# Optimization experiments

Measured on AMD Instinct MI355X. Metric: run time of the kernel, lower is better.

## Reference

```python
import jax, jax.numpy as jnp
import numpy as np

B, S, D, H, E = 4, 2048, 512, 8, 4  # batch, seq, embed, heads, expand
HD = D // H


def setup_inputs() -> dict:
    key = jax.random.key(0)
    ks = jax.random.split(key, 9)
    s = lambda k, shape, fan: jax.random.normal(k, shape, jnp.float32) * (fan ** -0.5)
    return {
        "x": jax.random.normal(ks[0], (B, S, D), jnp.float32),
        "Wq": s(ks[1], (D, D), D),
        "Wk": s(ks[2], (D, D), D),
        "Wv": s(ks[3], (D, D), D),
        "Wo": s(ks[4], (D, D), D),
        "W1": s(ks[5], (D, D * E), D),
        "b1": jnp.zeros((D * E,), jnp.float32),
        "W2": s(ks[6], (D * E, D), D * E),
        "b2": jnp.zeros((D,), jnp.float32),
    }


def _encoder_layer(x, Wq, Wk, Wv, Wo, W1, b1, W2, b2):
    # NOTE: source computes InstanceNorm1d twice but discards both results -> no-ops.
    scale = D ** -0.25  # applied to BOTH q and k (net 1/sqrt(embed_dim))
    q = (x @ Wq).reshape(B, S, H, HD).transpose(0, 2, 1, 3) * scale  # [B,H,S,hd]
    k = (x @ Wk).reshape(B, S, H, HD).transpose(0, 2, 1, 3) * scale
    v = (x @ Wv).reshape(B, S, H, HD).transpose(0, 2, 1, 3)
    scores = jnp.einsum('bhqd,bhkd->bhqk', q, k)  # [B,H,S,S]
    attn = jax.nn.softmax(scores, axis=-1)
    o = jnp.einsum('bhqk,bhkd->bhqd', attn, v)  # [B,H,S,hd]
    o = o.transpose(0, 2, 1, 3).reshape(B, S, D)
    x = o @ Wo + x  # residual 1
    h = jax.nn.gelu(x @ W1 + b1, approximate=True)  # torch GELU(approximate='tanh')
    return h @ W2 + b2 + x  # residual 2 (dropout=0, eval)


def reference(x, Wq, Wk, Wv, Wo, W1, b1, W2, b2):
    return _encoder_layer(x, Wq, Wk, Wv, Wo, W1, b1, W2, b2)
```

## Files before the change

### kernel.cpp

```cpp
#include <hip/hip_runtime.h>
#include <hip/hip_bf16.h>


typedef __bf16 bf16;
typedef __attribute__((ext_vector_type(8))) __bf16 bf16x8;
typedef __attribute__((ext_vector_type(4))) __bf16 bf16x4;
typedef __attribute__((ext_vector_type(4))) float f32x4;
typedef __attribute__((ext_vector_type(16))) float f32x16;
typedef __attribute__((ext_vector_type(2))) unsigned int u32x2;
typedef __attribute__((ext_vector_type(4))) unsigned int u32x4;

#define LOG2E 1.4426950408889634f
#define SCORE_SCALE 0.044194173824159216f
#define SCALE_L2E (SCORE_SCALE * LOG2E)
#define FIXED_M 12.0f

#if __has_builtin(__builtin_amdgcn_exp2f)
#define EXP2(x) __builtin_amdgcn_exp2f(x)
#else
#define EXP2(x) exp2f(x)
#endif

__device__ __forceinline__ void gl_lds16(const bf16* g, bf16* l) {
  __builtin_amdgcn_global_load_lds(
      (const __attribute__((address_space(1))) unsigned int*)g,
      (__attribute__((address_space(3))) unsigned int*)l, 16, 0, 0);
}

template <int N>
__device__ __forceinline__ void wait_vm_barrier() {
  if constexpr (N == 0)
    asm volatile("s_waitcnt vmcnt(0)\ns_barrier" ::: "memory");
  else if constexpr (N == 3)
    asm volatile("s_waitcnt vmcnt(3)\ns_barrier" ::: "memory");
  else if constexpr (N == 4)
    asm volatile("s_waitcnt vmcnt(4)\ns_barrier" ::: "memory");
}

__device__ __forceinline__ float gelu_tanh(float x) {
  float u = 0.7978845608028654f * (x + 0.044715f * x * x * x);
  float e = EXP2(u * (2.0f * LOG2E));
  float th = 1.0f - 2.0f / (e + 1.0f);
  return 0.5f * x * (1.0f + th);
}

__device__ __forceinline__ f32x4 mfma_bf16(bf16x8 a, bf16x8 b, f32x4 c) {
  return __builtin_amdgcn_mfma_f32_16x16x32_bf16(a, b, c, 0, 0, 0);
}
__device__ __forceinline__ f32x16 mfma32x16(bf16x8 a, bf16x8 b, f32x16 c) {
  return __builtin_amdgcn_mfma_f32_32x32x16_bf16(a, b, c, 0, 0, 0);
}

__device__ __forceinline__ void plswap(unsigned int& a, unsigned int& b) {
  asm volatile("v_permlane32_swap_b32 %0, %1" : "+v"(a), "+v"(b));
}

template <int MODE, typename OutT, int TN>
__global__ __launch_bounds__(256, 2) void gemm_bt(
    const bf16* __restrict__ A, const bf16* __restrict__ Bt,
    OutT* __restrict__ C, const float* __restrict__ bias,
    const float* __restrict__ resf, const bf16* __restrict__ resb,
    int M, int N, int K) {
  constexpr int MI = (TN == 128) ? 4 : 2;
  constexpr int L = (TN == 128) ? 4 : 3;
  __shared__ __align__(16) bf16 sA[3][128 * 32];
  __shared__ __align__(16) bf16 sB[3][TN * 32];
  const int tid = threadIdx.x;
  const int lane = tid & 63;
  const int quad = lane >> 4, lc = lane & 15;
  const int wave = tid >> 6;
  const int wr = (TN == 128) ? (wave >> 1) : wave;
  const int wc = (TN == 128) ? (wave & 1) : 0;
  const int m0 = blockIdx.y * 128, n0 = blockIdx.x * TN;

  const int srow = tid >> 2;
  const int kc = (tid & 3) * 8;
  const bf16* Ag1 = A + (size_t)(m0 + srow) * K + kc;
  const bf16* Ag2 = A + (size_t)(m0 + 64 + srow) * K + kc;
  const bf16* Bg1 = Bt + (size_t)(n0 + srow) * K + kc;
  const bf16* Bg2 = Bt + (size_t)(n0 + 64 + srow) * K + kc;
  const int o1 = tid * 8, o2 = (tid + 256) * 8;

  f32x4 acc[MI][4];
#pragma unroll
  for (int mi = 0; mi < MI; ++mi)
#pragma unroll
    for (int ni = 0; ni < 4; ++ni) acc[mi][ni] = (f32x4){0.f, 0.f, 0.f, 0.f};

  auto stage = [&](int t) {
    bf16* a = sA[t % 3];
    bf16* bb = sB[t % 3];
    gl_lds16(Ag1 + t * 32, a + o1);
    gl_lds16(Ag2 + t * 32, a + o2);
    gl_lds16(Bg1 + t * 32, bb + o1);
    if (TN == 128) gl_lds16(Bg2 + t * 32, bb + o2);
  };

  const int kIters = K >> 5;
  stage(0);
  stage(1);

  for (int kt = 0; kt < kIters; ++kt) {
    if (kt + 1 < kIters)
      wait_vm_barrier<L>();
    else
      wait_vm_barrier<0>();
    if (kt + 2 < kIters) stage(kt + 2);
    const bf16* cA = sA[kt % 3];
    const bf16* cB = sB[kt % 3];

    bf16x8 af[MI], bfm[4];
#pragma unroll
    for (int i = 0; i < MI; ++i)
      af[i] =
          *(const bf16x8*)(cA + ((wr * (16 * MI) + i * 16 + lc) * 32 + quad * 8));
#pragma unroll
    for (int i = 0; i < 4; ++i)
      bfm[i] = *(const bf16x8*)(cB + ((wc * 64 + i * 16 + lc) * 32 + quad * 8));
#pragma unroll
    for (int mi = 0; mi < MI; ++mi)
#pragma unroll
      for (int ni = 0; ni < 4; ++ni)
        acc[mi][ni] = mfma_bf16(af[mi], bfm[ni], acc[mi][ni]);
  }

#pragma unroll
  for (int mi = 0; mi < MI; ++mi) {
#pragma unroll
    for (int r = 0; r < 4; ++r) {
      const int row = m0 + wr * (16 * MI) + mi * 16 + quad * 4 + r;
#pragma unroll
      for (int ni = 0; ni < 4; ++ni) {
        const int col = n0 + wc * 64 + ni * 16 + lc;
        const size_t idx = (size_t)row * N + col;
        float v = acc[mi][ni][r];
        if (MODE == 1) v += resf[idx];
        if (MODE == 2) v = gelu_tanh(v + bias[col]);
        if (MODE == 3) v += bias[col] + (float)resb[idx];
        C[idx] = (OutT)v;
      }
    }
  }
}

__global__ __launch_bounds__(256, 2) void flash_attn(
    const bf16* __restrict__ QKV, const bf16* __restrict__ Vt,
    bf16* __restrict__ O) {
  const int tid = threadIdx.x;
  const int lane = tid & 63, wave = tid >> 6;
  const int lo5 = lane & 31, hi = lane >> 5;
  const int lin = blockIdx.y * 16 + blockIdx.x;
  const int xcd = lin & 7, slot = lin >> 3;
  const int bh = xcd * 4 + (slot >> 4);
  const int qt = slot & 15;
  const int b = bh >> 3, h = bh & 7;
  const int q0 = qt * 128 + wave * 32;

  __shared__ __align__(16) bf16 sK[3][4096];
  __shared__ __align__(16) bf16 sV[3][4096];

  const bf16* Qrow = QKV + (size_t)(b * 2048 + q0 + lo5) * 1536 + h * 64;
  bf16x8 qf[4];
#pragma unroll
  for (int i = 0; i < 4; ++i) qf[i] = *(const bf16x8*)(Qrow + i * 16 + hi * 8);

  const int colsw = (((lane & 7) ^ (lane >> 3)) << 3);
  const bf16* Kg0 = QKV + (size_t)b * 2048 * 1536 + 512 + (size_t)h * 64 +
                    (size_t)(wave * 16 + (lane >> 3)) * 1536 + colsw;
  const bf16* Vg0 = Vt + (size_t)bh * 64 * 2048 +
                    (size_t)(wave * 16 + (lane >> 3)) * 2048 + colsw;
  const int stag = wave * 1024;
  const int m7 = lo5 & 7;

  f32x16 oacc[2];
  oacc[0] = (f32x16)(0.f);
  oacc[1] = (f32x16)(0.f);
  float rs0 = 0.f, rs1 = 0.f, rs2 = 0.f, rs3 = 0.f;

  auto stage = [&](int t) {
    bf16* dk = sK[t % 3] + stag;
    bf16* dv = sV[t % 3] + stag;
    gl_lds16(Kg0 + (size_t)t * 64 * 1536, dk);
    gl_lds16(Kg0 + (size_t)(t * 64 + 8) * 1536, dk + 512);
    gl_lds16(Vg0 + t * 64, dv);
    gl_lds16(Vg0 + t * 64 + 8 * 2048, dv + 512);
  };
  stage(0);
  stage(1);

  for (int kt = 0; kt < 32; ++kt) {
    if (kt == 31)
      wait_vm_barrier<0>();
    else
      wait_vm_barrier<4>();
    if (kt + 2 < 32) stage(kt + 2);
    const bf16* cK = sK[kt % 3];
    const bf16* cV = sV[kt % 3];

    bf16x8 vf[2][4];
#pragma unroll
    for (int dh = 0; dh < 2; ++dh) {
      const int Rd = dh * 32 + lo5;
#pragma unroll
      for (int w = 0; w < 4; ++w)
        vf[dh][w] =
            *(const bf16x8*)(cV + Rd * 64 + (((2 * w + hi) ^ m7) << 3));
    }

    bf16x8 paw[4];
#pragma unroll
    for (int hl = 0; hl < 2; ++hl) {
      f32x16 st = (f32x16)(0.f);
      const int R = hl * 32 + lo5;
      __builtin_amdgcn_s_setprio(1);
#pragma unroll
      for (int i = 0; i < 4; ++i) {
        bf16x8 kf =
            *(const bf16x8*)(cK + R * 64 + (((2 * i + hi) ^ m7) << 3));
        st = mfma32x16(kf, qf[i], st);
      }
      __builtin_amdgcn_s_setprio(0);
      unsigned int q32[4][2];
#pragma unroll
      for (int g = 0; g < 4; ++g) {
        bf16x4 pb;
        float p0 = EXP2(st[4 * g + 0] * SCALE_L2E - FIXED_M);
        float p1 = EXP2(st[4 * g + 1] * SCALE_L2E - FIXED_M);
        float p2 = EXP2(st[4 * g + 2] * SCALE_L2E - FIXED_M);
        float p3 = EXP2(st[4 * g + 3] * SCALE_L2E - FIXED_M);
        rs0 += p0; rs1 += p1; rs2 += p2; rs3 += p3;
        pb[0] = (bf16)p0; pb[1] = (bf16)p1; pb[2] = (bf16)p2; pb[3] = (bf16)p3;
        u32x2 w2 = __builtin_bit_cast(u32x2, pb);
        q32[g][0] = w2[0];
        q32[g][1] = w2[1];
      }
#pragma unroll
      for (int t = 0; t < 2; ++t) {
        unsigned int a0 = q32[2 * t][0], a1 = q32[2 * t][1];
        unsigned int b0 = q32[2 * t + 1][0], b1 = q32[2 * t + 1][1];
        plswap(a0, b0);
        plswap(a1, b1);
        u32x4 f = {a0, a1, b0, b1};
        paw[hl * 2 + t] = __builtin_bit_cast(bf16x8, f);
      }
    }

    __builtin_amdgcn_s_setprio(1);
#pragma unroll
    for (int dh = 0; dh < 2; ++dh)
#pragma unroll
      for (int w = 0; w < 4; ++w)
        oacc[dh] = mfma32x16(paw[w], vf[dh][w], oacc[dh]);
    __builtin_amdgcn_s_setprio(0);
  }

  float rsum = (rs0 + rs1) + (rs2 + rs3);
  rsum += __shfl_xor(rsum, 32, 64);
  const size_t obase = (size_t)(b * 2048 + q0) * 512 + h * 64;
#pragma unroll
  for (int r = 0; r < 16; ++r) {
    const int qloc = (r & 3) + 8 * (r >> 2) + 4 * hi;
    const float inv = 1.0f / __shfl(rsum, qloc, 64);
#pragma unroll
    for (int dh = 0; dh < 2; ++dh)
      O[obase + (size_t)qloc * 512 + dh * 32 + lo5] =
          (bf16)(oacc[dh][r] * inv);
  }
}

__global__ __launch_bounds__(256) void prep(
    const float* __restrict__ x, const float* __restrict__ Wq,
    const float* __restrict__ Wk, const float* __restrict__ Wv,
    const float* __restrict__ Wo, const float* __restrict__ W1,
    const float* __restrict__ W2, bf16* __restrict__ xb,
    bf16* __restrict__ WqkvT, bf16* __restrict__ WoT, bf16* __restrict__ W1T,
    bf16* __restrict__ W2T) {
  const int bid = blockIdx.x;
  if (bid < 4096) {
    const size_t i = ((size_t)bid * 256 + threadIdx.x) * 4;
    const float4 v = *(const float4*)(x + i);
    bf16x4 o;
    o[0] = (bf16)v.x; o[1] = (bf16)v.y; o[2] = (bf16)v.z; o[3] = (bf16)v.w;
    *(bf16x4*)(xb + i) = o;
    return;
  }
  const int t = bid - 4096;
  const float* in;
  bf16* out;
  int in_ld, out_ld, bx, by;
  if (t < 1024) {
    const int q = t >> 8, r = t & 255;
    bx = r & 15; by = r >> 4; in_ld = 512; out_ld = 512;
    in = (q == 0) ? Wq : (q == 1) ? Wk : (q == 2) ? Wv : Wo;
    out = (q == 0) ? WqkvT
          : (q == 1) ? WqkvT + 512 * 512
          : (q == 2) ? WqkvT + 2 * 512 * 512
                     : WoT;
  } else if (t < 2048) {
    const int r = t - 1024;
    bx = r & 63; by = r >> 6; in_ld = 2048; out_ld = 512;
    in = W1; out = W1T;
  } else {
    const int r = t - 2048;
    bx = r & 15; by = r >> 4; in_ld = 512; out_ld = 2048;
    in = W2; out = W2T;
  }
  __shared__ __align__(16) bf16 tl[32][33];
  const int tx = threadIdx.x & 31, ty = threadIdx.x >> 5;
  const int n0 = bx * 32, k0 = by * 32;
#pragma unroll
  for (int i = 0; i < 4; ++i)
    tl[ty + 8 * i][tx] = (bf16)in[(size_t)(k0 + ty + 8 * i) * in_ld + n0 + tx];
  __syncthreads();
#pragma unroll
  for (int i = 0; i < 4; ++i)
    out[(size_t)(n0 + ty + 8 * i) * out_ld + k0 + tx] = tl[tx][ty + 8 * i];
}

__global__ __launch_bounds__(256) void transpose_v(
    const bf16* __restrict__ QKV, bf16* __restrict__ Vt) {
  __shared__ __align__(16) bf16 t[32][33];
  const int tx = threadIdx.x & 31, ty = threadIdx.x >> 5;
  const int bh = blockIdx.z, b = bh >> 3, h = bh & 7;
  const bf16* ip = QKV + (size_t)b * 2048 * 1536 + 1024 + h * 64;
  bf16* op = Vt + (size_t)bh * 64 * 2048;
  const int d0 = blockIdx.x * 32, s0 = blockIdx.y * 32;
#pragma unroll
  for (int i = 0; i < 4; ++i)
    t[ty + 8 * i][tx] = ip[(size_t)(s0 + ty + 8 * i) * 1536 + d0 + tx];
  __syncthreads();
#pragma unroll
  for (int i = 0; i < 4; ++i)
    op[(size_t)(d0 + ty + 8 * i) * 2048 + s0 + tx] = t[tx][ty + 8 * i];
}

extern "C" void kernel_launch(void* const* d_in, const int* in_sizes, int n_in,
                              void* d_out, int out_size, void* d_ws,
                              size_t ws_size, hipStream_t stream) {
  const float* x = (const float*)d_in[0];
  const float* Wq = (const float*)d_in[1];
  const float* Wk = (const float*)d_in[2];
  const float* Wv = (const float*)d_in[3];
  const float* Wo = (const float*)d_in[4];
  const float* W1 = (const float*)d_in[5];
  const float* b1 = (const float*)d_in[6];
  const float* W2 = (const float*)d_in[7];
  const float* b2 = (const float*)d_in[8];
  float* out = (float*)d_out;

  char* ws = (char*)d_ws;
  size_t off = 0;
  auto alloc = [&](size_t bytes) {
    char* p = ws + off;
    off += (bytes + 255) & ~(size_t)255;
    return p;
  };
  bf16* WqkvT = (bf16*)alloc(1536ULL * 512 * 2);
  bf16* WoT = (bf16*)alloc(512ULL * 512 * 2);
  bf16* W1T = (bf16*)alloc(2048ULL * 512 * 2);
  bf16* W2T = (bf16*)alloc(512ULL * 2048 * 2);
  bf16* xb = (bf16*)alloc(8192ULL * 512 * 2);
  bf16* QKV = (bf16*)alloc(8192ULL * 1536 * 2);
  bf16* Vt = (bf16*)alloc(32ULL * 64 * 2048 * 2);
  bf16* attn = (bf16*)alloc(8192ULL * 512 * 2);
  bf16* x2 = xb;
  bf16* hbuf = QKV;

  const dim3 tb(256);
  prep<<<dim3(7168), tb, 0, stream>>>(x, Wq, Wk, Wv, Wo, W1, W2, xb, WqkvT,
                                      WoT, W1T, W2T);
  gemm_bt<0, bf16, 128><<<dim3(12, 64), tb, 0, stream>>>(
      xb, WqkvT, QKV, nullptr, nullptr, nullptr, 8192, 1536, 512);
  transpose_v<<<dim3(2, 64, 32), tb, 0, stream>>>(QKV, Vt);
  flash_attn<<<dim3(16, 32), tb, 0, stream>>>(QKV, Vt, attn);
  gemm_bt<1, bf16, 64><<<dim3(8, 64), tb, 0, stream>>>(
      attn, WoT, x2, nullptr, x, nullptr, 8192, 512, 512);
  gemm_bt<2, bf16, 128><<<dim3(16, 64), tb, 0, stream>>>(
      x2, W1T, hbuf, b1, nullptr, nullptr, 8192, 2048, 512);
  gemm_bt<3, float, 64><<<dim3(8, 64), tb, 0, stream>>>(
      hbuf, W2T, out, b2, nullptr, x2, 8192, 512, 2048);
}
```

Baseline: 257.5 us.

## Fuse V transpose into QKV GEMM epilogue and double-buffer 128-wide GEMM tiles

The QKV projection GEMM now writes the V columns directly in transposed [B,H,hd,S] layout from its accumulators, which removes the separate transpose_v kernel launch and its extra read and write of V. Separately, the TN=128 GEMM path switches from a 3-stage LDS ring with vmcnt waits to a 2-buffer double-buffered loop with __syncthreads, which reduces LDS use and may raise occupancy. The cost is a full barrier every K step, with less lookahead on the loads. The transposed V stores are 4-element bf16 writes strided by the sequence length, so they may be poorly coalesced.

Result: faster. 247.0 us (-4.1%).

```diff
diff --git a/kernel.cpp b/kernel.cpp
--- a/kernel.cpp
+++ b/kernel.cpp
@@ -60,11 +60,11 @@
     const bf16* __restrict__ A, const bf16* __restrict__ Bt,
     OutT* __restrict__ C, const float* __restrict__ bias,
     const float* __restrict__ resf, const bf16* __restrict__ resb,
-    int M, int N, int K) {
+    bf16* __restrict__ vt, int M, int N, int K) {
   constexpr int MI = (TN == 128) ? 4 : 2;
-  constexpr int L = (TN == 128) ? 4 : 3;
-  __shared__ __align__(16) bf16 sA[3][128 * 32];
-  __shared__ __align__(16) bf16 sB[3][TN * 32];
+  constexpr int NBUF = (TN == 128) ? 2 : 3;
+  __shared__ __align__(16) bf16 sA[NBUF][128 * 32];
+  __shared__ __align__(16) bf16 sB[NBUF][TN * 32];
   const int tid = threadIdx.x;
   const int lane = tid & 63;
   const int quad = lane >> 4, lc = lane & 15;
@@ -87,43 +87,96 @@
 #pragma unroll
     for (int ni = 0; ni < 4; ++ni) acc[mi][ni] = (f32x4){0.f, 0.f, 0.f, 0.f};
 
-  auto stage = [&](int t) {
-    bf16* a = sA[t % 3];
-    bf16* bb = sB[t % 3];
-    gl_lds16(Ag1 + t * 32, a + o1);
-    gl_lds16(Ag2 + t * 32, a + o2);
-    gl_lds16(Bg1 + t * 32, bb + o1);
-    if (TN == 128) gl_lds16(Bg2 + t * 32, bb + o2);
-  };
-
   const int kIters = K >> 5;
-  stage(0);
-  stage(1);
-
-  for (int kt = 0; kt < kIters; ++kt) {
-    if (kt + 1 < kIters)
-      wait_vm_barrier<L>();
-    else
-      wait_vm_barrier<0>();
-    if (kt + 2 < kIters) stage(kt + 2);
-    const bf16* cA = sA[kt % 3];
-    const bf16* cB = sB[kt % 3];
-
-    bf16x8 af[MI], bfm[4];
-#pragma unroll
-    for (int i = 0; i < MI; ++i)
-      af[i] =
-          *(const bf16x8*)(cA + ((wr * (16 * MI) + i * 16 + lc) * 32 + quad * 8));
-#pragma unroll
-    for (int i = 0; i < 4; ++i)
-      bfm[i] = *(const bf16x8*)(cB + ((wc * 64 + i * 16 + lc) * 32 + quad * 8));
-#pragma unroll
-    for (int mi = 0; mi < MI; ++mi)
-#pragma unroll
-      for (int ni = 0; ni < 4; ++ni)
-        acc[mi][ni] = mfma_bf16(af[mi], bfm[ni], acc[mi][ni]);
-  }
-
+
+  if constexpr (TN == 128) {
+    gl_lds16(Ag1, sA[0] + o1);
+    gl_lds16(Ag2, sA[0] + o2);
+    gl_lds16(Bg1, sB[0] + o1);
+    gl_lds16(Bg2, sB[0] + o2);
+    Ag1 += 32; Ag2 += 32; Bg1 += 32; Bg2 += 32;
+
+    for (int kt = 0; kt < kIters; ++kt) {
+      __syncthreads();
+      const bf16* cA = sA[kt & 1];
+      const bf16* cB = sB[kt & 1];
+      if (kt + 1 < kIters) {
+        bf16* nA = sA[(kt + 1) & 1];
+        bf16* nB = sB[(kt + 1) & 1];
+        gl_lds16(Ag1, nA + o1);
+        gl_lds16(Ag2, nA + o2);
+        gl_lds16(Bg1, nB + o1);
+        gl_lds16(Bg2, nB + o2);
+        Ag1 += 32; Ag2 += 32; Bg1 += 32; Bg2 += 32;
+      }
+      bf16x8 af[MI], bfm[4];
+#pragma unroll
+      for (int i = 0; i < MI; ++i)
+        af[i] = *(const bf16x8*)(cA +
+                                 ((wr * 64 + i * 16 + lc) * 32 + quad * 8));
+#pragma unroll
+      for (int i = 0; i < 4; ++i)
+        bfm[i] =
+            *(const bf16x8*)(cB + ((wc * 64 + i * 16 + lc) * 32 + quad * 8));
+#pragma unroll
+      for (int mi = 0; mi < MI; ++mi)
+#pragma unroll
+        for (int ni = 0; ni < 4; ++ni)
+          acc[mi][ni] = mfma_bf16(af[mi], bfm[ni], acc[mi][ni]);
+    }
+  } else {
+    auto stage = [&](int t) {
+      bf16* a = sA[t % 3];
+      bf16* bb = sB[t % 3];
+      gl_lds16(Ag1 + t * 32, a + o1);
+      gl_lds16(Ag2 + t * 32, a + o2);
+      gl_lds16(Bg1 + t * 32, bb + o1);
+    };
+    stage(0);
+    stage(1);
+    for (int kt = 0; kt < kIters; ++kt) {
+      if (kt + 1 < kIters)
+        wait_vm_barrier<3>();
+      else
+        wait_vm_barrier<0>();
+      if (kt + 2 < kIters) stage(kt + 2);
+      const bf16* cA = sA[kt % 3];
+      const bf16* cB = sB[kt % 3];
+      bf16x8 af[MI], bfm[4];
+#pragma unroll
+      for (int i = 0; i < MI; ++i)
+        af[i] = *(const bf16x8*)(cA +
+                                 ((wr * 32 + i * 16 + lc) * 32 + quad * 8));
+#pragma unroll
+      for (int i = 0; i < 4; ++i)
+        bfm[i] = *(const bf16x8*)(cB + ((i * 16 + lc) * 32 + quad * 8));
+#pragma unroll
+      for (int mi = 0; mi < MI; ++mi)
+#pragma unroll
+        for (int ni = 0; ni < 4; ++ni)
+          acc[mi][ni] = mfma_bf16(af[mi], bfm[ni], acc[mi][ni]);
+    }
+  }
+
+  if constexpr (MODE == 0) {
+    if (n0 >= 1024) {
+#pragma unroll
+      for (int mi = 0; mi < MI; ++mi) {
+        const int row0 = m0 + wr * (16 * MI) + mi * 16 + quad * 4;
+        const int bb = row0 >> 11, s0 = row0 & 2047;
+#pragma unroll
+        for (int ni = 0; ni < 4; ++ni) {
+          const int col = n0 + wc * 64 + ni * 16 + lc;
+          const int hh = (col >> 6) & 7, d = col & 63;
+          bf16x4 pb;
+#pragma unroll
+          for (int r = 0; r < 4; ++r) pb[r] = (bf16)acc[mi][ni][r];
+          *(bf16x4*)(vt + ((size_t)((bb * 8 + hh) * 64 + d)) * 2048 + s0) = pb;
+        }
+      }
+      return;
+    }
+  }
 #pragma unroll
   for (int mi = 0; mi < MI; ++mi) {
 #pragma unroll
@@ -317,23 +370,6 @@
     out[(size_t)(n0 + ty + 8 * i) * out_ld + k0 + tx] = tl[tx][ty + 8 * i];
 }
 
-__global__ __launch_bounds__(256) void transpose_v(
-    const bf16* __restrict__ QKV, bf16* __restrict__ Vt) {
-  __shared__ __align__(16) bf16 t[32][33];
-  const int tx = threadIdx.x & 31, ty = threadIdx.x >> 5;
-  const int bh = blockIdx.z, b = bh >> 3, h = bh & 7;
-  const bf16* ip = QKV + (size_t)b * 2048 * 1536 + 1024 + h * 64;
-  bf16* op = Vt + (size_t)bh * 64 * 2048;
-  const int d0 = blockIdx.x * 32, s0 = blockIdx.y * 32;
-#pragma unroll
-  for (int i = 0; i < 4; ++i)
-    t[ty + 8 * i][tx] = ip[(size_t)(s0 + ty + 8 * i) * 1536 + d0 + tx];
-  __syncthreads();
-#pragma unroll
-  for (int i = 0; i < 4; ++i)
-    op[(size_t)(d0 + ty + 8 * i) * 2048 + s0 + tx] = t[tx][ty + 8 * i];
-}
-
 extern "C" void kernel_launch(void* const* d_in, const int* in_sizes, int n_in,
                               void* d_out, int out_size, void* d_ws,
                               size_t ws_size, hipStream_t stream) {
@@ -370,13 +406,12 @@
   prep<<<dim3(7168), tb, 0, stream>>>(x, Wq, Wk, Wv, Wo, W1, W2, xb, WqkvT,
                                       WoT, W1T, W2T);
   gemm_bt<0, bf16, 128><<<dim3(12, 64), tb, 0, stream>>>(
-      xb, WqkvT, QKV, nullptr, nullptr, nullptr, 8192, 1536, 512);
-  transpose_v<<<dim3(2, 64, 32), tb, 0, stream>>>(QKV, Vt);
+      xb, WqkvT, QKV, nullptr, nullptr, nullptr, Vt, 8192, 1536, 512);
   flash_attn<<<dim3(16, 32), tb, 0, stream>>>(QKV, Vt, attn);
   gemm_bt<1, bf16, 64><<<dim3(8, 64), tb, 0, stream>>>(
-      attn, WoT, x2, nullptr, x, nullptr, 8192, 512, 512);
+      attn, WoT, x2, nullptr, x, nullptr, nullptr, 8192, 512, 512);
   gemm_bt<2, bf16, 128><<<dim3(16, 64), tb, 0, stream>>>(
-      x2, W1T, hbuf, b1, nullptr, nullptr, 8192, 2048, 512);
+      x2, W1T, hbuf, b1, nullptr, nullptr, nullptr, 8192, 2048, 512);
   gemm_bt<3, float, 64><<<dim3(8, 64), tb, 0, stream>>>(
-      hbuf, W2T, out, b2, nullptr, x2, 8192, 512, 2048);
-}
+      hbuf, W2T, out, b2, nullptr, x2, nullptr, 8192, 512, 2048);
+}
```
